# Optimization experiments

Measured on AMD Instinct MI355X. Metric: run time of the kernel, lower is better.

## Reference

```python
import jax, jax.numpy as jnp
import numpy as np

DIM = 320
NUM_HEADS = 5
HEAD_DIM = DIM // NUM_HEADS  # 64
SCALE = HEAD_DIM ** -0.5


def setup_inputs() -> dict:
    key = jax.random.key(0)
    k1, k2, k3, k4 = jax.random.split(key, 4)
    B, N, C = 8, 2048, DIM
    x = jax.random.normal(k1, (B, N, C), dtype=jnp.float32)
    # nn.Linear(dim, dim*3, bias=False): weight [3*dim, dim]
    w_qkv = jax.random.normal(k2, (3 * C, C), dtype=jnp.float32) * (C ** -0.5)
    # nn.Linear(dim, dim): weight [dim, dim], bias [dim]
    w_proj = jax.random.normal(k3, (C, C), dtype=jnp.float32) * (C ** -0.5)
    b_proj = jax.random.normal(k4, (C,), dtype=jnp.float32) * 0.01
    return {"x": x, "w_qkv": w_qkv, "w_proj": w_proj, "b_proj": b_proj}


def reference(x, w_qkv, w_proj, b_proj):
    B, N, C = x.shape
    H, D = NUM_HEADS, HEAD_DIM
    # qkv projection: [B, N, 3C] -> [3, B, H, N, D]
    qkv = jnp.einsum('bnc,kc->bnk', x, w_qkv)
    qkv = qkv.reshape(B, N, 3, H, D).transpose(2, 0, 3, 1, 4)
    q, k, v = qkv[0], qkv[1], qkv[2]
    # full attention matrix [B, H, N, N] (retained by original module)
    attn = jnp.einsum('bhnd,bhmd->bhnm', q, k) * SCALE
    attn = jax.nn.softmax(attn, axis=-1)
    # attn_drop p=0 -> identity (eval/deterministic)
    out = jnp.einsum('bhnm,bhmd->bhnd', attn, v)
    out = out.transpose(0, 2, 1, 3).reshape(B, N, C)
    out = jnp.einsum('bnc,oc->bno', out, w_proj) + b_proj
    # proj_drop p=0 -> identity
    return out
```

## Files before the change

kernel.cpp:

```cpp
#include <hip/hip_runtime.h>
#include <hip/hip_bf16.h>


typedef __attribute__((ext_vector_type(8))) short bf16x8;
typedef __attribute__((ext_vector_type(4))) float f32x4;

#define MFMA(a, b, c) __builtin_amdgcn_mfma_f32_16x16x32_bf16((a), (b), (c), 0, 0, 0)

#define QSCALE 0.18033688322643216f

static __device__ __forceinline__ bf16x8 ld8(const __hip_bfloat16* p) {
    return *reinterpret_cast<const bf16x8*>(p);
}

static __device__ __forceinline__ void split_bf16(float v, __hip_bfloat16& h,
                                                  __hip_bfloat16& l) {
    __hip_bfloat16 hh = __float2bfloat16(v);
    h = hh;
    l = __float2bfloat16(v - __bfloat162float(hh));
}

__global__ __launch_bounds__(256)
void split_inputs(const float* __restrict__ x, const float* __restrict__ wq,
                  const float* __restrict__ wp,
                  __hip_bfloat16* __restrict__ xb, __hip_bfloat16* __restrict__ wqb,
                  __hip_bfloat16* __restrict__ wph, __hip_bfloat16* __restrict__ wpl)
{
    const size_t tid = (size_t)blockIdx.x * blockDim.x + threadIdx.x;
    const size_t stride = (size_t)gridDim.x * blockDim.x;
    const float4* x4 = (const float4*)x;
    ushort4* xb4 = (ushort4*)xb;
    for (size_t i = tid; i < 1310720u; i += stride) {
        float4 v = x4[i];
        __hip_bfloat16 b0 = __float2bfloat16(v.x), b1 = __float2bfloat16(v.y);
        __hip_bfloat16 b2 = __float2bfloat16(v.z), b3 = __float2bfloat16(v.w);
        ushort4 u;
        u.x = *reinterpret_cast<unsigned short*>(&b0);
        u.y = *reinterpret_cast<unsigned short*>(&b1);
        u.z = *reinterpret_cast<unsigned short*>(&b2);
        u.w = *reinterpret_cast<unsigned short*>(&b3);
        xb4[i] = u;
    }
    for (size_t i = tid; i < 307200u; i += stride) wqb[i] = __float2bfloat16(wq[i]);
    for (size_t i = tid; i < 102400u; i += stride) split_bf16(wp[i], wph[i], wpl[i]);
}

__global__ __launch_bounds__(256)
void qkv_kernel(const __hip_bfloat16* __restrict__ x,
                const __hip_bfloat16* __restrict__ w,
                __hip_bfloat16* __restrict__ qout,
                __hip_bfloat16* __restrict__ kp,
                __hip_bfloat16* __restrict__ vp)
{
    __shared__ __align__(16) __hip_bfloat16 As[128 * 72];
    __shared__ __align__(16) __hip_bfloat16 Bs[64 * 72];

    const int tid  = threadIdx.x;
    const int wv   = tid >> 6;
    const int lane = tid & 63;
    const int quad = lane >> 4;
    const int col  = lane & 15;
    const int m0   = blockIdx.x * 128;
    const int n0   = blockIdx.y * 64;

    f32x4 acc[2][4];
#pragma unroll
    for (int i = 0; i < 2; ++i)
#pragma unroll
        for (int j = 0; j < 4; ++j) acc[i][j] = (f32x4){0.f, 0.f, 0.f, 0.f};

    for (int k0 = 0; k0 < 320; k0 += 64) {
        __syncthreads();
#pragma unroll
        for (int i = 0; i < 4; ++i) {
            int ch = tid + i * 256;
            int r = ch >> 3, sg = ch & 7;
            *reinterpret_cast<float4*>(&As[r * 72 + sg * 8]) =
                *reinterpret_cast<const float4*>(&x[(m0 + r) * 320 + k0 + sg * 8]);
        }
#pragma unroll
        for (int i = 0; i < 2; ++i) {
            int ch = tid + i * 256;
            int r = ch >> 3, sg = ch & 7;
            *reinterpret_cast<float4*>(&Bs[r * 72 + sg * 8]) =
                *reinterpret_cast<const float4*>(&w[(n0 + r) * 320 + k0 + sg * 8]);
        }
        __syncthreads();

#pragma unroll
        for (int hf = 0; hf < 2; ++hf) {
            bf16x8 a0 = ld8(&As[(wv * 32 + col) * 72 + hf * 32 + quad * 8]);
            bf16x8 a1 = ld8(&As[(wv * 32 + 16 + col) * 72 + hf * 32 + quad * 8]);
#pragma unroll
            for (int nt = 0; nt < 4; ++nt) {
                bf16x8 b = ld8(&Bs[(nt * 16 + col) * 72 + hf * 32 + quad * 8]);
                acc[0][nt] = MFMA(a0, b, acc[0][nt]);
                acc[1][nt] = MFMA(a1, b, acc[1][nt]);
            }
        }
    }

    const int s = blockIdx.y / 5;
    const int h = blockIdx.y % 5;
#pragma unroll
    for (int mt = 0; mt < 2; ++mt) {
#pragma unroll
        for (int nt = 0; nt < 4; ++nt) {
#pragma unroll
            for (int r = 0; r < 4; ++r) {
                int m = m0 + wv * 32 + mt * 16 + quad * 4 + r;
                int d = nt * 16 + col;
                int b = m >> 11, n = m & 2047;
                int bh = b * 5 + h;
                float val = acc[mt][nt][r];
                if (s == 0) {
                    qout[((size_t)bh * 2048 + n) * 64 + d] =
                        __float2bfloat16(val * QSCALE);
                } else if (s == 1) {
                    int p = n >> 6, nn = n & 63;
                    size_t a = ((size_t)(bh * 32 + p) * 8 + (d >> 5) * 4 + (nn >> 4)) * 512
                             + (((d >> 3) & 3) * 16 + (nn & 15)) * 8 + (d & 7);
                    kp[a] = __float2bfloat16(val);
                } else {
                    int p = n >> 6;
                    size_t a = ((size_t)(bh * 32 + p) * 8 + ((n >> 5) & 1) * 4 + (d >> 4)) * 512
                             + (((n >> 3) & 3) * 16 + (d & 15)) * 8 + (n & 7);
                    vp[a] = __float2bfloat16(val);
                }
            }
        }
    }
}

__global__ __launch_bounds__(128)
void attn_kernel(const __hip_bfloat16* __restrict__ Q,
                 const __hip_bfloat16* __restrict__ Kp,
                 const __hip_bfloat16* __restrict__ Vp,
                 __hip_bfloat16* __restrict__ A2h,
                 __hip_bfloat16* __restrict__ A2l)
{
    __shared__ __align__(16) unsigned char smraw[9216];

    const int tid  = threadIdx.x;
    const int wv   = tid >> 6;
    const int lane = tid & 63;
    const int quad = lane >> 4;
    const int col  = lane & 15;
    const int bh = blockIdx.y, b = bh / 5, h = bh % 5;
    const int q0 = blockIdx.x * 32;
    const int t0 = wv * 16;

    __hip_bfloat16* Ps = (__hip_bfloat16*)smraw + wv * 2304;
    __hip_bfloat16* ps_w = Ps + (quad * 4) * 72 + col;
    const __hip_bfloat16* ps_r = Ps + col * 72 + quad * 8;

    const __hip_bfloat16* kt = Kp + (size_t)bh * 131072 + (size_t)t0 * 4096 + lane * 8;
    const __hip_bfloat16* vt = Vp + (size_t)bh * 131072 + (size_t)t0 * 4096 + lane * 8;
    const __hip_bfloat16* Qh = Q + (size_t)bh * 131072;

    bf16x8 qf[2][2];
#pragma unroll
    for (int mt = 0; mt < 2; ++mt)
#pragma unroll
        for (int hf = 0; hf < 2; ++hf)
            qf[mt][hf] = ld8(&Qh[(q0 + mt * 16 + col) * 64 + hf * 32 + quad * 8]);

    f32x4 lp[2];
    f32x4 o[2][4];
#pragma unroll
    for (int mt = 0; mt < 2; ++mt) {
        lp[mt] = (f32x4){0.f, 0.f, 0.f, 0.f};
#pragma unroll
        for (int dt = 0; dt < 4; ++dt) o[mt][dt] = (f32x4){0.f, 0.f, 0.f, 0.f};
    }

    bf16x8 ka[8];
#pragma unroll
    for (int f = 0; f < 8; ++f) ka[f] = ld8(kt + f * 512);
    kt += 4096;

    for (int t = 0; t < 16; ++t) {
        f32x4 s[2][4];
#pragma unroll
        for (int mt = 0; mt < 2; ++mt)
#pragma unroll
            for (int nt = 0; nt < 4; ++nt) {
                f32x4 z = (f32x4){0.f, 0.f, 0.f, 0.f};
                z = MFMA(qf[mt][0], ka[nt], z);
                z = MFMA(qf[mt][1], ka[4 + nt], z);
                s[mt][nt] = z;
            }

        bf16x8 va[8];
#pragma unroll
        for (int f = 0; f < 8; ++f) va[f] = ld8(vt + f * 512);
        vt += 4096;

#pragma unroll
        for (int f = 0; f < 8; ++f) ka[f] = ld8(kt + f * 512);
        kt += 4096;

#pragma unroll
        for (int mt = 0; mt < 2; ++mt)
#pragma unroll
            for (int nt = 0; nt < 4; ++nt) {
                f32x4 pv;
#pragma unroll
                for (int r = 0; r < 4; ++r)
                    pv[r] = __builtin_amdgcn_exp2f(s[mt][nt][r]);
                lp[mt] += pv;
#pragma unroll
                for (int r = 0; r < 4; ++r)
                    ps_w[(mt * 16 + r) * 72 + nt * 16] = __float2bfloat16(pv[r]);
            }
        __asm__ volatile("s_waitcnt lgkmcnt(0)" ::: "memory");

#pragma unroll
        for (int mt = 0; mt < 2; ++mt)
#pragma unroll
            for (int kk = 0; kk < 2; ++kk) {
                bf16x8 pf = ld8(ps_r + mt * 1152 + kk * 32);
#pragma unroll
                for (int dt = 0; dt < 4; ++dt)
                    o[mt][dt] = MFMA(pf, va[kk * 4 + dt], o[mt][dt]);
            }
    }

    float lval[2][4];
#pragma unroll
    for (int mt = 0; mt < 2; ++mt)
#pragma unroll
        for (int r = 0; r < 4; ++r) {
            float v = lp[mt][r];
#pragma unroll
            for (int off = 1; off < 16; off <<= 1)
                v += __shfl_xor(v, off, 64);
            lval[mt][r] = v;
        }

    float* cbo = (float*)smraw;
    float* cbl = cbo + 2048;
    __syncthreads();
    if (wv == 1) {
#pragma unroll
        for (int mt = 0; mt < 2; ++mt)
#pragma unroll
            for (int dt = 0; dt < 4; ++dt)
#pragma unroll
                for (int r = 0; r < 4; ++r)
                    cbo[(mt * 16 + quad * 4 + r) * 64 + dt * 16 + col] = o[mt][dt][r];
        if (col == 0)
#pragma unroll
            for (int mt = 0; mt < 2; ++mt)
#pragma unroll
                for (int r = 0; r < 4; ++r)
                    cbl[mt * 16 + quad * 4 + r] = lval[mt][r];
    }
    __syncthreads();
    if (wv == 0) {
#pragma unroll
        for (int mt = 0; mt < 2; ++mt) {
#pragma unroll
            for (int r = 0; r < 4; ++r) {
                int row = mt * 16 + quad * 4 + r;
                float inv = 1.0f / (lval[mt][r] + cbl[row]);
                int grow = q0 + row;
#pragma unroll
                for (int dt = 0; dt < 4; ++dt) {
                    int d = dt * 16 + col;
                    float val = (o[mt][dt][r] + cbo[row * 64 + d]) * inv;
                    size_t idx = ((size_t)(b * 2048 + grow)) * 320 + h * 64 + d;
                    split_bf16(val, A2h[idx], A2l[idx]);
                }
            }
        }
    }
}

__global__ __launch_bounds__(256)
void proj_kernel(const __hip_bfloat16* __restrict__ ah, const __hip_bfloat16* __restrict__ al,
                 const __hip_bfloat16* __restrict__ wh, const __hip_bfloat16* __restrict__ wl,
                 const float* __restrict__ bias,
                 float* __restrict__ out)
{
    __shared__ __align__(16) __hip_bfloat16 Ash[128 * 40];
    __shared__ __align__(16) __hip_bfloat16 Asl[128 * 40];
    __shared__ __align__(16) __hip_bfloat16 Bsh[64 * 40];
    __shared__ __align__(16) __hip_bfloat16 Bsl[64 * 40];

    const int tid  = threadIdx.x;
    const int wv   = tid >> 6;
    const int lane = tid & 63;
    const int quad = lane >> 4;
    const int col  = lane & 15;
    const int m0   = blockIdx.x * 128;
    const int n0   = blockIdx.y * 64;

    f32x4 acc[2][4];
#pragma unroll
    for (int i = 0; i < 2; ++i)
#pragma unroll
        for (int j = 0; j < 4; ++j) acc[i][j] = (f32x4){0.f, 0.f, 0.f, 0.f};

    for (int k0 = 0; k0 < 320; k0 += 32) {
        __syncthreads();
#pragma unroll
        for (int i = 0; i < 2; ++i) {
            int ch = tid + i * 256;
            int r = ch >> 2, sg = ch & 3;
            *reinterpret_cast<float4*>(&Ash[r * 40 + sg * 8]) =
                *reinterpret_cast<const float4*>(&ah[(m0 + r) * 320 + k0 + sg * 8]);
            *reinterpret_cast<float4*>(&Asl[r * 40 + sg * 8]) =
                *reinterpret_cast<const float4*>(&al[(m0 + r) * 320 + k0 + sg * 8]);
        }
        {
            int r = tid >> 2, sg = tid & 3;
            *reinterpret_cast<float4*>(&Bsh[r * 40 + sg * 8]) =
                *reinterpret_cast<const float4*>(&wh[(n0 + r) * 320 + k0 + sg * 8]);
            *reinterpret_cast<float4*>(&Bsl[r * 40 + sg * 8]) =
                *reinterpret_cast<const float4*>(&wl[(n0 + r) * 320 + k0 + sg * 8]);
        }
        __syncthreads();

        bf16x8 a0h = ld8(&Ash[(wv * 32 + col) * 40 + quad * 8]);
        bf16x8 a1h = ld8(&Ash[(wv * 32 + 16 + col) * 40 + quad * 8]);
        bf16x8 a0l = ld8(&Asl[(wv * 32 + col) * 40 + quad * 8]);
        bf16x8 a1l = ld8(&Asl[(wv * 32 + 16 + col) * 40 + quad * 8]);
#pragma unroll
        for (int nt = 0; nt < 4; ++nt) {
            bf16x8 bh = ld8(&Bsh[(nt * 16 + col) * 40 + quad * 8]);
            bf16x8 bl = ld8(&Bsl[(nt * 16 + col) * 40 + quad * 8]);
            acc[0][nt] = MFMA(a0h, bh, acc[0][nt]);
            acc[0][nt] = MFMA(a0h, bl, acc[0][nt]);
            acc[0][nt] = MFMA(a0l, bh, acc[0][nt]);
            acc[1][nt] = MFMA(a1h, bh, acc[1][nt]);
            acc[1][nt] = MFMA(a1h, bl, acc[1][nt]);
            acc[1][nt] = MFMA(a1l, bh, acc[1][nt]);
        }
    }

#pragma unroll
    for (int nt = 0; nt < 4; ++nt) {
        float bv = bias[n0 + nt * 16 + col];
#pragma unroll
        for (int mt = 0; mt < 2; ++mt) {
#pragma unroll
            for (int r = 0; r < 4; ++r) {
                int m = m0 + wv * 32 + mt * 16 + quad * 4 + r;
                out[(size_t)m * 320 + n0 + nt * 16 + col] = acc[mt][nt][r] + bv;
            }
        }
    }
}

extern "C" void kernel_launch(void* const* d_in, const int* in_sizes, int n_in,
                              void* d_out, int out_size, void* d_ws, size_t ws_size,
                              hipStream_t stream)
{
    const float* x      = (const float*)d_in[0];
    const float* w_qkv  = (const float*)d_in[1];
    const float* w_proj = (const float*)d_in[2];
    const float* b_proj = (const float*)d_in[3];
    float* out = (float*)d_out;

    const size_t NX = 5242880, NWQ = 307200, NWP = 102400;
    __hip_bfloat16* xb  = (__hip_bfloat16*)d_ws;
    __hip_bfloat16* wqb = xb + NX;
    __hip_bfloat16* wph = wqb + NWQ;
    __hip_bfloat16* wpl = wph + NWP;
    __hip_bfloat16* q   = wpl + NWP;
    __hip_bfloat16* kp  = q + NX;
    __hip_bfloat16* vp  = kp + NX;
    __hip_bfloat16* a2l = vp + NX;
    __hip_bfloat16* a2h = xb;

    split_inputs<<<1024, 256, 0, stream>>>(x, w_qkv, w_proj, xb, wqb, wph, wpl);
    qkv_kernel<<<dim3(128, 15), 256, 0, stream>>>(xb, wqb, q, kp, vp);
    attn_kernel<<<dim3(64, 40), 128, 0, stream>>>(q, kp, vp, a2h, a2l);
    proj_kernel<<<dim3(128, 5), 256, 0, stream>>>(a2h, a2l, wph, wpl, b_proj, out);
}
```

Before: 190.8 us.

## Fuse fp32-to-bf16 conversion into GEMM loads and drop split-bf16 projection

Removes the separate split_inputs kernel. The qkv and proj GEMMs now read fp32 x and the weights directly and convert them to bf16 while staging into shared memory. The attention output is stored as a single bf16 value instead of a hi/lo pair, and the projection GEMM becomes a plain bf16 GEMM with a K tile of 64 instead of the three-MFMA split-precision scheme. This saves one launch and a full pass over x, halves proj traffic and MFMA work, and lowers projection accuracy. The GEMM prologue now reads twice the bytes per element of x.

```diff
diff --git a/kernel.cpp b/kernel.cpp
--- a/kernel.cpp
+++ b/kernel.cpp
@@ -13,41 +13,25 @@
     return *reinterpret_cast<const bf16x8*>(p);
 }
 
-static __device__ __forceinline__ void split_bf16(float v, __hip_bfloat16& h,
-                                                  __hip_bfloat16& l) {
-    __hip_bfloat16 hh = __float2bfloat16(v);
-    h = hh;
-    l = __float2bfloat16(v - __bfloat162float(hh));
+static __device__ __forceinline__ unsigned short bfbits(float v) {
+    __hip_bfloat16 b = __float2bfloat16(v);
+    return *reinterpret_cast<unsigned short*>(&b);
+}
+
+static __device__ __forceinline__ bf16x8 cvt8(const float* src) {
+    float4 a = *reinterpret_cast<const float4*>(src);
+    float4 b = *reinterpret_cast<const float4*>(src + 4);
+    bf16x8 v;
+    v[0] = (short)bfbits(a.x); v[1] = (short)bfbits(a.y);
+    v[2] = (short)bfbits(a.z); v[3] = (short)bfbits(a.w);
+    v[4] = (short)bfbits(b.x); v[5] = (short)bfbits(b.y);
+    v[6] = (short)bfbits(b.z); v[7] = (short)bfbits(b.w);
+    return v;
 }
 
 __global__ __launch_bounds__(256)
-void split_inputs(const float* __restrict__ x, const float* __restrict__ wq,
-                  const float* __restrict__ wp,
-                  __hip_bfloat16* __restrict__ xb, __hip_bfloat16* __restrict__ wqb,
-                  __hip_bfloat16* __restrict__ wph, __hip_bfloat16* __restrict__ wpl)
-{
-    const size_t tid = (size_t)blockIdx.x * blockDim.x + threadIdx.x;
-    const size_t stride = (size_t)gridDim.x * blockDim.x;
-    const float4* x4 = (const float4*)x;
-    ushort4* xb4 = (ushort4*)xb;
-    for (size_t i = tid; i < 1310720u; i += stride) {
-        float4 v = x4[i];
-        __hip_bfloat16 b0 = __float2bfloat16(v.x), b1 = __float2bfloat16(v.y);
-        __hip_bfloat16 b2 = __float2bfloat16(v.z), b3 = __float2bfloat16(v.w);
-        ushort4 u;
-        u.x = *reinterpret_cast<unsigned short*>(&b0);
-        u.y = *reinterpret_cast<unsigned short*>(&b1);
-        u.z = *reinterpret_cast<unsigned short*>(&b2);
-        u.w = *reinterpret_cast<unsigned short*>(&b3);
-        xb4[i] = u;
-    }
-    for (size_t i = tid; i < 307200u; i += stride) wqb[i] = __float2bfloat16(wq[i]);
-    for (size_t i = tid; i < 102400u; i += stride) split_bf16(wp[i], wph[i], wpl[i]);
-}
-
-__global__ __launch_bounds__(256)
-void qkv_kernel(const __hip_bfloat16* __restrict__ x,
-                const __hip_bfloat16* __restrict__ w,
+void qkv_kernel(const float* __restrict__ x,
+                const float* __restrict__ w,
                 __hip_bfloat16* __restrict__ qout,
                 __hip_bfloat16* __restrict__ kp,
                 __hip_bfloat16* __restrict__ vp)
@@ -75,15 +59,15 @@
         for (int i = 0; i < 4; ++i) {
             int ch = tid + i * 256;
             int r = ch >> 3, sg = ch & 7;
-            *reinterpret_cast<float4*>(&As[r * 72 + sg * 8]) =
-                *reinterpret_cast<const float4*>(&x[(m0 + r) * 320 + k0 + sg * 8]);
+            *reinterpret_cast<bf16x8*>(&As[r * 72 + sg * 8]) =
+                cvt8(&x[(m0 + r) * 320 + k0 + sg * 8]);
         }
 #pragma unroll
         for (int i = 0; i < 2; ++i) {
             int ch = tid + i * 256;
             int r = ch >> 3, sg = ch & 7;
-            *reinterpret_cast<float4*>(&Bs[r * 72 + sg * 8]) =
-                *reinterpret_cast<const float4*>(&w[(n0 + r) * 320 + k0 + sg * 8]);
+            *reinterpret_cast<bf16x8*>(&Bs[r * 72 + sg * 8]) =
+                cvt8(&w[(n0 + r) * 320 + k0 + sg * 8]);
         }
         __syncthreads();
 
@@ -136,8 +120,7 @@
 void attn_kernel(const __hip_bfloat16* __restrict__ Q,
                  const __hip_bfloat16* __restrict__ Kp,
                  const __hip_bfloat16* __restrict__ Vp,
-                 __hip_bfloat16* __restrict__ A2h,
-                 __hip_bfloat16* __restrict__ A2l)
+                 __hip_bfloat16* __restrict__ A2)
 {
     __shared__ __align__(16) unsigned char smraw[9216];
 
@@ -269,8 +252,8 @@
                 for (int dt = 0; dt < 4; ++dt) {
                     int d = dt * 16 + col;
                     float val = (o[mt][dt][r] + cbo[row * 64 + d]) * inv;
-                    size_t idx = ((size_t)(b * 2048 + grow)) * 320 + h * 64 + d;
-                    split_bf16(val, A2h[idx], A2l[idx]);
+                    A2[((size_t)(b * 2048 + grow)) * 320 + h * 64 + d] =
+                        __float2bfloat16(val);
                 }
             }
         }
@@ -278,15 +261,13 @@
 }
 
 __global__ __launch_bounds__(256)
-void proj_kernel(const __hip_bfloat16* __restrict__ ah, const __hip_bfloat16* __restrict__ al,
-                 const __hip_bfloat16* __restrict__ wh, const __hip_bfloat16* __restrict__ wl,
+void proj_kernel(const __hip_bfloat16* __restrict__ a2,
+                 const float* __restrict__ w,
                  const float* __restrict__ bias,
                  float* __restrict__ out)
 {
-    __shared__ __align__(16) __hip_bfloat16 Ash[128 * 40];
-    __shared__ __align__(16) __hip_bfloat16 Asl[128 * 40];
-    __shared__ __align__(16) __hip_bfloat16 Bsh[64 * 40];
-    __shared__ __align__(16) __hip_bfloat16 Bsl[64 * 40];
+    __shared__ __align__(16) __hip_bfloat16 As[128 * 72];
+    __shared__ __align__(16) __hip_bfloat16 Bs[64 * 72];
 
     const int tid  = threadIdx.x;
     const int wv   = tid >> 6;
@@ -302,40 +283,34 @@
 #pragma unroll
         for (int j = 0; j < 4; ++j) acc[i][j] = (f32x4){0.f, 0.f, 0.f, 0.f};
 
-    for (int k0 = 0; k0 < 320; k0 += 32) {
+    for (int k0 = 0; k0 < 320; k0 += 64) {
         __syncthreads();
+#pragma unroll
+        for (int i = 0; i < 4; ++i) {
+            int ch = tid + i * 256;
+            int r = ch >> 3, sg = ch & 7;
+            *reinterpret_cast<float4*>(&As[r * 72 + sg * 8]) =
+                *reinterpret_cast<const float4*>(&a2[(m0 + r) * 320 + k0 + sg * 8]);
+        }
 #pragma unroll
         for (int i = 0; i < 2; ++i) {
             int ch = tid + i * 256;
-            int r = ch >> 2, sg = ch & 3;
-            *reinterpret_cast<float4*>(&Ash[r * 40 + sg * 8]) =
-                *reinterpret_cast<const float4*>(&ah[(m0 + r) * 320 + k0 + sg * 8]);
-            *reinterpret_cast<float4*>(&Asl[r * 40 + sg * 8]) =
-                *reinterpret_cast<const float4*>(&al[(m0 + r) * 320 + k0 + sg * 8]);
-        }
-        {
-            int r = tid >> 2, sg = tid & 3;
-            *reinterpret_cast<float4*>(&Bsh[r * 40 + sg * 8]) =
-                *reinterpret_cast<const float4*>(&wh[(n0 + r) * 320 + k0 + sg * 8]);
-            *reinterpret_cast<float4*>(&Bsl[r * 40 + sg * 8]) =
-                *reinterpret_cast<const float4*>(&wl[(n0 + r) * 320 + k0 + sg * 8]);
+            int r = ch >> 3, sg = ch & 7;
+            *reinterpret_cast<bf16x8*>(&Bs[r * 72 + sg * 8]) =
+                cvt8(&w[(n0 + r) * 320 + k0 + sg * 8]);
         }
         __syncthreads();
 
-        bf16x8 a0h = ld8(&Ash[(wv * 32 + col) * 40 + quad * 8]);
-        bf16x8 a1h = ld8(&Ash[(wv * 32 + 16 + col) * 40 + quad * 8]);
-        bf16x8 a0l = ld8(&Asl[(wv * 32 + col) * 40 + quad * 8]);
-        bf16x8 a1l = ld8(&Asl[(wv * 32 + 16 + col) * 40 + quad * 8]);
-#pragma unroll
-        for (int nt = 0; nt < 4; ++nt) {
-            bf16x8 bh = ld8(&Bsh[(nt * 16 + col) * 40 + quad * 8]);
-            bf16x8 bl = ld8(&Bsl[(nt * 16 + col) * 40 + quad * 8]);
-            acc[0][nt] = MFMA(a0h, bh, acc[0][nt]);
-            acc[0][nt] = MFMA(a0h, bl, acc[0][nt]);
-            acc[0][nt] = MFMA(a0l, bh, acc[0][nt]);
-            acc[1][nt] = MFMA(a1h, bh, acc[1][nt]);
-            acc[1][nt] = MFMA(a1h, bl, acc[1][nt]);
-            acc[1][nt] = MFMA(a1l, bh, acc[1][nt]);
+#pragma unroll
+        for (int hf = 0; hf < 2; ++hf) {
+            bf16x8 a0 = ld8(&As[(wv * 32 + col) * 72 + hf * 32 + quad * 8]);
+            bf16x8 a1 = ld8(&As[(wv * 32 + 16 + col) * 72 + hf * 32 + quad * 8]);
+#pragma unroll
+            for (int nt = 0; nt < 4; ++nt) {
+                bf16x8 b = ld8(&Bs[(nt * 16 + col) * 72 + hf * 32 + quad * 8]);
+                acc[0][nt] = MFMA(a0, b, acc[0][nt]);
+                acc[1][nt] = MFMA(a1, b, acc[1][nt]);
+            }
         }
     }
 
@@ -363,19 +338,13 @@
     const float* b_proj = (const float*)d_in[3];
     float* out = (float*)d_out;
 
-    const size_t NX = 5242880, NWQ = 307200, NWP = 102400;
-    __hip_bfloat16* xb  = (__hip_bfloat16*)d_ws;
-    __hip_bfloat16* wqb = xb + NX;
-    __hip_bfloat16* wph = wqb + NWQ;
-    __hip_bfloat16* wpl = wph + NWP;
-    __hip_bfloat16* q   = wpl + NWP;
-    __hip_bfloat16* kp  = q + NX;
-    __hip_bfloat16* vp  = kp + NX;
-    __hip_bfloat16* a2l = vp + NX;
-    __hip_bfloat16* a2h = xb;
-
-    split_inputs<<<1024, 256, 0, stream>>>(x, w_qkv, w_proj, xb, wqb, wph, wpl);
-    qkv_kernel<<<dim3(128, 15), 256, 0, stream>>>(xb, wqb, q, kp, vp);
-    attn_kernel<<<dim3(64, 40), 128, 0, stream>>>(q, kp, vp, a2h, a2l);
-    proj_kernel<<<dim3(128, 5), 256, 0, stream>>>(a2h, a2l, wph, wpl, b_proj, out);
-}
+    const size_t NX = 5242880;
+    __hip_bfloat16* q  = (__hip_bfloat16*)d_ws;
+    __hip_bfloat16* kp = q + NX;
+    __hip_bfloat16* vp = kp + NX;
+    __hip_bfloat16* a2 = vp + NX;
+
+    qkv_kernel<<<dim3(128, 15), 256, 0, stream>>>(x, w_qkv, q, kp, vp);
+    attn_kernel<<<dim3(64, 40), 128, 0, stream>>>(q, kp, vp, a2);
+    proj_kernel<<<dim3(128, 5), 256, 0, stream>>>(a2, w_proj, b_proj, out);
+}
```

Measured after the change: 196.8 us. 1.03x slower.
